# Optimization experiments

Measured on AMD Instinct MI355X. Metric: run time of the kernel, lower is better.

## Reference

```python
import jax, jax.numpy as jnp
import numpy as np

ALPHA = 50.0
BETA = 0.5
EPS = 1e-6

def setup_inputs() -> dict:
    key = jax.random.key(0)
    k1, k2, k3 = jax.random.split(key, 3)
    N, D = 131072, 512
    output1 = jax.random.normal(k1, (N, D), dtype=jnp.float32)
    output2 = jax.random.normal(k2, (N, D), dtype=jnp.float32)
    target = jax.random.randint(k3, (N,), 0, 2, dtype=jnp.int64)
    return {"output1": output1, "output2": output2, "target": target}

def reference(output1, output2, target):
    # per-pair cosine similarity (torch.nn.CosineSimilarity, dim=1, eps=1e-6)
    dot = jnp.sum(output1 * output2, axis=1)
    denom = jnp.maximum(jnp.linalg.norm(output1, axis=1) * jnp.linalg.norm(output2, axis=1), EPS)
    d = dot / denom  # [N]
    # binomial deviance terms
    pos = (2.0 / BETA) * jax.nn.softplus(-BETA * (d - 0.5))
    neg = (2.0 / ALPHA) * jax.nn.softplus(ALPHA * (d - 2.0))
    is_pos = (target == 1)
    num_pos = jnp.sum(is_pos)
    num_neg = target.shape[0] - num_pos
    pos_loss = jnp.sum(jnp.where(is_pos, pos, 0.0)) / jnp.maximum(num_pos, 1)
    neg_loss = jnp.sum(jnp.where(is_pos, 0.0, neg)) / jnp.maximum(num_neg, 1)
    return pos_loss + neg_loss
```

## Files before the change

kernel.cpp:

```cpp
#include <hip/hip_runtime.h>
#include <math.h>

#define N_ROWS 131072
#define D 512
#define BLOCKS 4096
#define ALPHA 50.0f
#define BETA 0.5f
#define EPS 1e-6f

__device__ __forceinline__ float softplusf(float x) {
    if (x > 0.0f) return x + log1pf(__expf(-x));
    return log1pf(__expf(x));
}

__global__ __launch_bounds__(256) void binloss_main(
    const float* __restrict__ o1, const float* __restrict__ o2,
    const int* __restrict__ target,
    float* __restrict__ sums ,
    int* __restrict__ cnt ) {

    const int lane = threadIdx.x & 63;
    const int wave = threadIdx.x >> 6;
    const int gwave = blockIdx.x * 4 + wave;
    const int nwaves = gridDim.x * 4;

    float posAcc = 0.0f, negAcc = 0.0f;
    int posCnt = 0;

    for (int row = gwave; row < N_ROWS; row += nwaves) {
        const float4* p1 = (const float4*)(o1 + (size_t)row * D);
        const float4* p2 = (const float4*)(o2 + (size_t)row * D);
        float4 a0 = p1[lane];
        float4 a1 = p1[lane + 64];
        float4 b0 = p2[lane];
        float4 b1 = p2[lane + 64];

        float dot = a0.x * b0.x + a0.y * b0.y + a0.z * b0.z + a0.w * b0.w
                  + a1.x * b1.x + a1.y * b1.y + a1.z * b1.z + a1.w * b1.w;
        float s1  = a0.x * a0.x + a0.y * a0.y + a0.z * a0.z + a0.w * a0.w
                  + a1.x * a1.x + a1.y * a1.y + a1.z * a1.z + a1.w * a1.w;
        float s2  = b0.x * b0.x + b0.y * b0.y + b0.z * b0.z + b0.w * b0.w
                  + b1.x * b1.x + b1.y * b1.y + b1.z * b1.z + b1.w * b1.w;

        #pragma unroll
        for (int off = 32; off > 0; off >>= 1) {
            dot += __shfl_xor(dot, off);
            s1  += __shfl_xor(s1, off);
            s2  += __shfl_xor(s2, off);
        }

        if (lane == 0) {
            float denom = fmaxf(sqrtf(s1) * sqrtf(s2), EPS);
            float d = dot / denom;
            int t = target[row];
            if (t == 1) {
                posAcc += (2.0f / BETA) * softplusf(-BETA * (d - 0.5f));
                posCnt++;
            } else {
                negAcc += (2.0f / ALPHA) * softplusf(ALPHA * (d - 2.0f));
            }
        }
    }

    __shared__ float sPos[4], sNeg[4];
    __shared__ int sCnt[4];
    if (lane == 0) {
        sPos[wave] = posAcc;
        sNeg[wave] = negAcc;
        sCnt[wave] = posCnt;
    }
    __syncthreads();
    if (threadIdx.x == 0) {
        float p = sPos[0] + sPos[1] + sPos[2] + sPos[3];
        float n = sNeg[0] + sNeg[1] + sNeg[2] + sNeg[3];
        int c = sCnt[0] + sCnt[1] + sCnt[2] + sCnt[3];
        atomicAdd(&sums[0], p);
        atomicAdd(&sums[1], n);
        atomicAdd(&cnt[0], c);
    }
}

__global__ void binloss_final(const float* __restrict__ sums,
                              const int* __restrict__ cnt,
                              float* __restrict__ out) {
    int np = cnt[0];
    int nn = N_ROWS - np;
    float pos_loss = sums[0] / (float)(np > 1 ? np : 1);
    float neg_loss = sums[1] / (float)(nn > 1 ? nn : 1);
    out[0] = pos_loss + neg_loss;
}

extern "C" void kernel_launch(void* const* d_in, const int* in_sizes, int n_in,
                              void* d_out, int out_size, void* d_ws, size_t ws_size,
                              hipStream_t stream) {
    const float* o1 = (const float*)d_in[0];
    const float* o2 = (const float*)d_in[1];
    const int* tgt = (const int*)d_in[2];
    float* out = (float*)d_out;
    float* sums = (float*)d_ws;
    int* cnt = (int*)((char*)d_ws + 2 * sizeof(float));

    hipMemsetAsync(d_ws, 0, 16, stream);

    binloss_main<<<BLOCKS, 256, 0, stream>>>(o1, o2, tgt, sums, cnt);
    binloss_final<<<1, 1, 0, stream>>>(sums, cnt, out);
}
```

Measured before the change: 575.7 us.

## Batch four rows per wave iteration and fuse final reduction via last-block counter

```diff
diff --git a/kernel.cpp b/kernel.cpp
--- a/kernel.cpp
+++ b/kernel.cpp
@@ -4,6 +4,10 @@
 #define N_ROWS 131072
 #define D 512
 #define BLOCKS 4096
+#define WAVES_PER_BLOCK 4
+#define ROWS_PER_WAVE (N_ROWS / (BLOCKS * WAVES_PER_BLOCK))
+#define R_PER_IT 4
+#define N_IT (ROWS_PER_WAVE / R_PER_IT)
 #define ALPHA 50.0f
 #define BETA 0.5f
 #define EPS 1e-6f
@@ -17,53 +21,67 @@
     const float* __restrict__ o1, const float* __restrict__ o2,
     const int* __restrict__ target,
     float* __restrict__ sums ,
-    int* __restrict__ cnt ) {
+    int* __restrict__ icnt ,
+    unsigned int* __restrict__ done,
+    float* __restrict__ out) {
 
     const int lane = threadIdx.x & 63;
     const int wave = threadIdx.x >> 6;
-    const int gwave = blockIdx.x * 4 + wave;
-    const int nwaves = gridDim.x * 4;
+    const int gwave = blockIdx.x * WAVES_PER_BLOCK + wave;
+    const int rowBase = gwave * ROWS_PER_WAVE;
 
     float posAcc = 0.0f, negAcc = 0.0f;
     int posCnt = 0;
 
-    for (int row = gwave; row < N_ROWS; row += nwaves) {
-        const float4* p1 = (const float4*)(o1 + (size_t)row * D);
-        const float4* p2 = (const float4*)(o2 + (size_t)row * D);
-        float4 a0 = p1[lane];
-        float4 a1 = p1[lane + 64];
-        float4 b0 = p2[lane];
-        float4 b1 = p2[lane + 64];
+    #pragma unroll
+    for (int it = 0; it < N_IT; ++it) {
+        const int row = rowBase + it * R_PER_IT;
+        float dot[R_PER_IT], s1[R_PER_IT], s2[R_PER_IT];
 
-        float dot = a0.x * b0.x + a0.y * b0.y + a0.z * b0.z + a0.w * b0.w
-                  + a1.x * b1.x + a1.y * b1.y + a1.z * b1.z + a1.w * b1.w;
-        float s1  = a0.x * a0.x + a0.y * a0.y + a0.z * a0.z + a0.w * a0.w
-                  + a1.x * a1.x + a1.y * a1.y + a1.z * a1.z + a1.w * a1.w;
-        float s2  = b0.x * b0.x + b0.y * b0.y + b0.z * b0.z + b0.w * b0.w
-                  + b1.x * b1.x + b1.y * b1.y + b1.z * b1.z + b1.w * b1.w;
+        #pragma unroll
+        for (int r = 0; r < R_PER_IT; ++r) {
+            const float4* p1 = (const float4*)(o1 + (size_t)(row + r) * D);
+            const float4* p2 = (const float4*)(o2 + (size_t)(row + r) * D);
+            float4 a0 = p1[lane];
+            float4 a1 = p1[lane + 64];
+            float4 b0 = p2[lane];
+            float4 b1 = p2[lane + 64];
+            dot[r] = a0.x * b0.x + a0.y * b0.y + a0.z * b0.z + a0.w * b0.w
+                   + a1.x * b1.x + a1.y * b1.y + a1.z * b1.z + a1.w * b1.w;
+            s1[r]  = a0.x * a0.x + a0.y * a0.y + a0.z * a0.z + a0.w * a0.w
+                   + a1.x * a1.x + a1.y * a1.y + a1.z * a1.z + a1.w * a1.w;
+            s2[r]  = b0.x * b0.x + b0.y * b0.y + b0.z * b0.z + b0.w * b0.w
+                   + b1.x * b1.x + b1.y * b1.y + b1.z * b1.z + b1.w * b1.w;
+        }
 
         #pragma unroll
         for (int off = 32; off > 0; off >>= 1) {
-            dot += __shfl_xor(dot, off);
-            s1  += __shfl_xor(s1, off);
-            s2  += __shfl_xor(s2, off);
+            #pragma unroll
+            for (int r = 0; r < R_PER_IT; ++r) {
+                dot[r] += __shfl_xor(dot[r], off);
+                s1[r]  += __shfl_xor(s1[r], off);
+                s2[r]  += __shfl_xor(s2[r], off);
+            }
         }
 
         if (lane == 0) {
-            float denom = fmaxf(sqrtf(s1) * sqrtf(s2), EPS);
-            float d = dot / denom;
-            int t = target[row];
-            if (t == 1) {
-                posAcc += (2.0f / BETA) * softplusf(-BETA * (d - 0.5f));
-                posCnt++;
-            } else {
-                negAcc += (2.0f / ALPHA) * softplusf(ALPHA * (d - 2.0f));
+            #pragma unroll
+            for (int r = 0; r < R_PER_IT; ++r) {
+                float denom = fmaxf(sqrtf(s1[r]) * sqrtf(s2[r]), EPS);
+                float d = dot[r] / denom;
+                int t = target[row + r];
+                if (t == 1) {
+                    posAcc += (2.0f / BETA) * softplusf(-BETA * (d - 0.5f));
+                    posCnt++;
+                } else {
+                    negAcc += (2.0f / ALPHA) * softplusf(ALPHA * (d - 2.0f));
+                }
             }
         }
     }
 
-    __shared__ float sPos[4], sNeg[4];
-    __shared__ int sCnt[4];
+    __shared__ float sPos[WAVES_PER_BLOCK], sNeg[WAVES_PER_BLOCK];
+    __shared__ int sCnt[WAVES_PER_BLOCK];
     if (lane == 0) {
         sPos[wave] = posAcc;
         sNeg[wave] = negAcc;
@@ -76,18 +94,20 @@
         int c = sCnt[0] + sCnt[1] + sCnt[2] + sCnt[3];
         atomicAdd(&sums[0], p);
         atomicAdd(&sums[1], n);
-        atomicAdd(&cnt[0], c);
+        atomicAdd(&icnt[0], c);
+        __threadfence();
+        unsigned int old = atomicAdd(done, 1u);
+        if (old == (unsigned int)(gridDim.x - 1)) {
+            __threadfence();
+            float ps = __hip_atomic_load(&sums[0], __ATOMIC_RELAXED, __HIP_MEMORY_SCOPE_AGENT);
+            float ns = __hip_atomic_load(&sums[1], __ATOMIC_RELAXED, __HIP_MEMORY_SCOPE_AGENT);
+            int np = __hip_atomic_load(&icnt[0], __ATOMIC_RELAXED, __HIP_MEMORY_SCOPE_AGENT);
+            int nn = N_ROWS - np;
+            float pos_loss = ps / (float)(np > 1 ? np : 1);
+            float neg_loss = ns / (float)(nn > 1 ? nn : 1);
+            out[0] = pos_loss + neg_loss;
+        }
     }
-}
-
-__global__ void binloss_final(const float* __restrict__ sums,
-                              const int* __restrict__ cnt,
-                              float* __restrict__ out) {
-    int np = cnt[0];
-    int nn = N_ROWS - np;
-    float pos_loss = sums[0] / (float)(np > 1 ? np : 1);
-    float neg_loss = sums[1] / (float)(nn > 1 ? nn : 1);
-    out[0] = pos_loss + neg_loss;
 }
 
 extern "C" void kernel_launch(void* const* d_in, const int* in_sizes, int n_in,
@@ -99,9 +119,9 @@
     float* out = (float*)d_out;
     float* sums = (float*)d_ws;
     int* cnt = (int*)((char*)d_ws + 2 * sizeof(float));
+    unsigned int* done = (unsigned int*)((char*)d_ws + 3 * sizeof(float));
 
     hipMemsetAsync(d_ws, 0, 16, stream);
 
-    binloss_main<<<BLOCKS, 256, 0, stream>>>(o1, o2, tgt, sums, cnt);
-    binloss_final<<<1, 1, 0, stream>>>(sums, cnt, out);
+    binloss_main<<<BLOCKS, 256, 0, stream>>>(o1, o2, tgt, sums, cnt, done, out);
 }
```

New measurement: 696.5 us. +21.0%, slower.
